# Kernel optimization log

Measured on AMD Instinct MI355X. Metric: run time of the kernel, lower is better.

Reference implementation:

```python
import jax, jax.numpy as jnp
import numpy as np

NUM_HOPS = 3

def _position_encoding(sentence_size, embedding_size):
    # Vectorized version of the double loop in the source.
    i = np.arange(1, embedding_size + 1, dtype=np.float32)[:, None]  # [E,1]
    j = np.arange(1, sentence_size + 1, dtype=np.float32)[None, :]   # [1,S]
    enc = (i - embedding_size / 2.0) * (j - sentence_size / 2.0)
    enc = 1.0 + 4.0 * enc / embedding_size / sentence_size
    return jnp.asarray(np.transpose(enc))  # [S, E]

def setup_inputs() -> dict:
    key = jax.random.key(0)
    ks = jax.random.split(key, 9)
    B, M, S, E, V, OUT = 16, 512, 32, 128, 32000, 128
    scale = 0.02
    return {
        "queries": jax.random.randint(ks[0], (B, S), 0, V, dtype=jnp.int32),
        "stories": jax.random.randint(ks[1], (B, M, S), 0, V, dtype=jnp.int32),
        "query_biases": jax.random.normal(ks[2], (V - 1, E), jnp.float32) * scale,
        "stories_biases": jax.random.normal(ks[3], (V - 1, E), jnp.float32) * scale,
        "memory_biases": jax.random.normal(ks[4], (M, E), jnp.float32) * scale,
        "output_biases": jax.random.normal(ks[5], (V - 1, E), jnp.float32) * scale,
        "w_intermediate": jax.random.normal(ks[6], (E, E), jnp.float32) * scale,
        "w_output": jax.random.normal(ks[7], (E, OUT), jnp.float32) * scale,
        "w_final": jax.random.normal(ks[8], (OUT, V), jnp.float32) * scale,
    }

def reference(queries, stories, query_biases, stories_biases, memory_biases,
              output_biases, w_intermediate, w_output, w_final):
    B, M, S = stories.shape
    E = query_biases.shape[1]
    enc = _position_encoding(S, E)  # [S, E]
    nil = jnp.zeros((1, E), dtype=query_biases.dtype)

    # Story memory: gather -> positional weight -> reduce over sentence axis.
    st_tab = jnp.concatenate([stories_biases, nil], axis=0)          # [V, E]
    mem_emb = st_tab[stories]                                        # [B,M,S,E]
    memory = jnp.einsum('bmse,se->bme', mem_emb, enc) + memory_biases

    # Query embedding.
    q_tab = jnp.concatenate([query_biases, nil], axis=0)
    q = jnp.einsum('bse,se->be', q_tab[queries], enc)                # [B,E]

    # Output memory.
    o_tab = jnp.concatenate([output_biases, nil], axis=0)
    output = jnp.einsum('bmse,se->bme', o_tab[stories], enc)         # [B,M,E]

    out_layer = q
    for hop in range(NUM_HOPS):
        probs = jax.nn.softmax(jnp.einsum('bme,be->bm', memory, q))  # [B,M]
        layer_out = jnp.einsum('bme,bm->be', output, probs)          # [B,E]
        w = w_output if hop == NUM_HOPS - 1 else w_intermediate
        out_layer = (q + layer_out) @ w
        q = out_layer                     # pre-nonlinearity state, as in source
        out_layer = jax.nn.relu(out_layer)

    return out_layer @ w_final            # [B, vocab]
```

## Files before the change

kernel.cpp:

```cpp
#include <hip/hip_runtime.h>

constexpr int kB  = 16;
constexpr int kM  = 512;
constexpr int kS  = 32;
constexpr int kE  = 128;
constexpr int kV  = 32000;
constexpr int kVN = kV - 1;
constexpr int kMS = 132;

__global__ __launch_bounds__(256) void embed_stories_kernel(
    const int*   __restrict__ stories,
    const float* __restrict__ st_bias,
    const float* __restrict__ out_bias,
    const float* __restrict__ mem_bias,
    float*       __restrict__ memory,
    float*       __restrict__ output,
    unsigned*    __restrict__ bar)
{
    __shared__ int sidx[2][kS];
    __shared__ __align__(16) float pm[8][kE];
    __shared__ __align__(16) float po[8][kE];

    const int t    = threadIdx.x;
    const int row0 = blockIdx.x * 2;
    if (t < 64) sidx[t >> 5][t & 31] = stories[row0 * kS + t];
    if (blockIdx.x == 0 && t < kB) bar[t] = 0u;
    __syncthreads();

    const int g    = t >> 5;
    const int lane = t & 31;
    const int p    = g >> 2;
    const int ph   = g & 3;
    const int e0   = lane * 4;
    const float ef0 = (float)(e0 - 63), ef1 = (float)(e0 - 62);
    const float ef2 = (float)(e0 - 61), ef3 = (float)(e0 - 60);

    float4 am = {0.f, 0.f, 0.f, 0.f};
    float4 ao = {0.f, 0.f, 0.f, 0.f};
    #pragma unroll
    for (int j = 0; j < 8; ++j) {
        const int s   = ph * 8 + j;
        const int idx = sidx[p][s];
        const int ci  = idx < kVN ? idx : (kVN - 1);
        const float live = (idx < kVN) ? 1.0f : 0.0f;
        const float sf = (float)(s - 15) * (1.0f / 1024.0f);
        const float4 vm = *(const float4*)(st_bias  + (size_t)ci * kE + e0);
        const float4 vo = *(const float4*)(out_bias + (size_t)ci * kE + e0);
        const float c0 = fmaf(ef0, sf, 1.0f) * live;
        const float c1 = fmaf(ef1, sf, 1.0f) * live;
        const float c2 = fmaf(ef2, sf, 1.0f) * live;
        const float c3 = fmaf(ef3, sf, 1.0f) * live;
        am.x = fmaf(vm.x, c0, am.x); am.y = fmaf(vm.y, c1, am.y);
        am.z = fmaf(vm.z, c2, am.z); am.w = fmaf(vm.w, c3, am.w);
        ao.x = fmaf(vo.x, c0, ao.x); ao.y = fmaf(vo.y, c1, ao.y);
        ao.z = fmaf(vo.z, c2, ao.z); ao.w = fmaf(vo.w, c3, ao.w);
    }
    *(float4*)&pm[g][e0] = am;
    *(float4*)&po[g][e0] = ao;
    __syncthreads();

    const int pr = t >> 7;
    const int e  = t & 127;
    const int row = row0 + pr;
    const int m   = row & (kM - 1);
    const float sm = pm[pr * 4 + 0][e] + pm[pr * 4 + 1][e] +
                     pm[pr * 4 + 2][e] + pm[pr * 4 + 3][e];
    const float so = po[pr * 4 + 0][e] + po[pr * 4 + 1][e] +
                     po[pr * 4 + 2][e] + po[pr * 4 + 3][e];
    memory[(size_t)row * kE + e] = sm + mem_bias[m * kE + e];
    output[(size_t)row * kE + e] = so;
}

__device__ __forceinline__ void group_barrier(unsigned* ctr, unsigned target)
{
    __syncthreads();
    if (threadIdx.x == 0) {
        __hip_atomic_fetch_add(ctr, 1u, __ATOMIC_RELEASE, __HIP_MEMORY_SCOPE_AGENT);
        while (__hip_atomic_load(ctr, __ATOMIC_RELAXED, __HIP_MEMORY_SCOPE_AGENT) < target)
            __builtin_amdgcn_s_sleep(2);
    }
    __syncthreads();
}
__device__ __forceinline__ void cstore(float* p, float v) {
    __hip_atomic_store(p, v, __ATOMIC_RELAXED, __HIP_MEMORY_SCOPE_AGENT);
}
__device__ __forceinline__ float cload(const float* p) {
    return __hip_atomic_load(p, __ATOMIC_RELAXED, __HIP_MEMORY_SCOPE_AGENT);
}

__global__ __launch_bounds__(1024) void hops_kernel(
    const int*   __restrict__ queries,
    const float* __restrict__ q_bias,
    const float* __restrict__ memory,
    const float* __restrict__ output,
    const float* __restrict__ w_int,
    const float* __restrict__ w_out,
    float*       __restrict__ numer,
    float*       __restrict__ denom,
    float*       __restrict__ xg,
    unsigned*    __restrict__ bar)
{
    __shared__ __align__(16) float mem_lds[128 * kMS];
    __shared__ __align__(16) float out_lds[128 * kE];
    __shared__ float sc_q[128];
    __shared__ __align__(16) float q_s[kE];
    __shared__ float xb[kE];
    __shared__ __align__(16) float part8[8][kE];
    __shared__ int qidx[kS];

    const int bid = blockIdx.x;
    const int b   = bid & 15;
    const int qtr = bid >> 4;
    const int t   = threadIdx.x;
    unsigned* ctr = bar + b;

    const float* memb = memory + ((size_t)b * kM + qtr * 128) * kE;
    const float* outb = output + ((size_t)b * kM + qtr * 128) * kE;
    #pragma unroll
    for (int i = 0; i < 4; ++i) {
        const int flat = t + i * 1024;
        const int rr = flat >> 5, ff = (flat & 31) * 4;
        *(float4*)&mem_lds[rr * kMS + ff] = *(const float4*)&memb[(size_t)rr * kE + ff];
        *(float4*)&out_lds[rr * kE  + ff] = *(const float4*)&outb[(size_t)rr * kE + ff];
    }
    if (t < kS) qidx[t] = queries[b * kS + t];
    __syncthreads();

    if (t < 256) {
        const int g = t >> 5, lane = t & 31, e0 = lane * 4;
        const float f0 = (float)(e0 - 63) * (1.0f / 1024.0f);
        const float f1 = (float)(e0 - 62) * (1.0f / 1024.0f);
        const float f2 = (float)(e0 - 61) * (1.0f / 1024.0f);
        const float f3 = (float)(e0 - 60) * (1.0f / 1024.0f);
        float4 a = {0.f, 0.f, 0.f, 0.f};
        #pragma unroll
        for (int j = 0; j < 4; ++j) {
            const int s   = g * 4 + j;
            const int idx = qidx[s];
            const int ci  = idx < kVN ? idx : (kVN - 1);
            const float live = (idx < kVN) ? 1.0f : 0.0f;
            const float sf = (float)(s - 15);
            const float4 v = *(const float4*)&q_bias[(size_t)ci * kE + e0];
            a.x = fmaf(v.x, fmaf(f0, sf, 1.f) * live, a.x);
            a.y = fmaf(v.y, fmaf(f1, sf, 1.f) * live, a.y);
            a.z = fmaf(v.z, fmaf(f2, sf, 1.f) * live, a.z);
            a.w = fmaf(v.w, fmaf(f3, sf, 1.f) * live, a.w);
        }
        *(float4*)&part8[g][e0] = a;
    }
    __syncthreads();
    if (t < kE) {
        float s = 0.f;
        #pragma unroll
        for (int g = 0; g < 8; ++g) s += part8[g][t];
        q_s[t] = s;
    }
    __syncthreads();

    const int grp = t >> 7;
    const int e   = t & 127;

    for (int hop = 0; hop < 3; ++hop) {
        {
            const int rw = t >> 3, sub = t & 7;
            const float4* qv = (const float4*)&q_s[sub * 16];
            const float4* mv = (const float4*)&mem_lds[rw * kMS + sub * 16];
            float d = 0.f;
            #pragma unroll
            for (int i = 0; i < 4; ++i) {
                const float4 m4 = mv[i], q4 = qv[i];
                d = fmaf(m4.x, q4.x, d); d = fmaf(m4.y, q4.y, d);
                d = fmaf(m4.z, q4.z, d); d = fmaf(m4.w, q4.w, d);
            }
            d += __shfl_down(d, 4);
            d += __shfl_down(d, 2);
            d += __shfl_down(d, 1);
            if (sub == 0) sc_q[rw] = __expf(d);
        }
        __syncthreads();

        {
            float acc = 0.f;
            const float* pp = &sc_q[grp * 16];
            const float* ob = &out_lds[grp * 16 * kE + e];
            #pragma unroll
            for (int j = 0; j < 16; ++j)
                acc = fmaf(pp[j], ob[j * kE], acc);
            part8[grp][e] = acc;
        }
        __syncthreads();

        const int pb = hop & 1;
        float* nq = numer + (((size_t)pb * kB + b) * 4 + qtr) * kE;
        if (t < kE) {
            float s = 0.f;
            #pragma unroll
            for (int g = 0; g < 8; ++g) s += part8[g][t];
            cstore(&nq[t], s);
        } else if (t < 192) {
            const int l = t - 128;
            float s2 = sc_q[l] + sc_q[l + 64];
            #pragma unroll
            for (int off = 32; off; off >>= 1) s2 += __shfl_down(s2, off);
            if (l == 0) cstore(&denom[((size_t)pb * kB + b) * 4 + qtr], s2);
        }

        group_barrier(ctr, 4u * (hop + 1));

        if (t < kE) {
            const float* nn = numer + ((size_t)pb * kB + b) * 4 * kE;
            const float* dd = denom + ((size_t)pb * kB + b) * 4;
            const float ns = cload(&nn[t]) + cload(&nn[kE + t]) +
                             cload(&nn[2 * kE + t]) + cload(&nn[3 * kE + t]);
            const float ds = cload(&dd[0]) + cload(&dd[1]) +
                             cload(&dd[2]) + cload(&dd[3]);
            xb[t] = q_s[t] + ns / ds;
        }
        __syncthreads();

        {
            const float* w = (hop == 2) ? w_out : w_int;
            float acc = 0.f;
            #pragma unroll
            for (int j = 0; j < 16; ++j) {
                const int k = grp * 16 + j;
                acc = fmaf(xb[k], w[k * kE + e], acc);
            }
            part8[grp][e] = acc;
        }
        __syncthreads();
        if (t < kE) {
            float s = 0.f;
            #pragma unroll
            for (int g = 0; g < 8; ++g) s += part8[g][t];
            q_s[t] = s;
        }
        __syncthreads();
    }

    if (qtr == 0 && t < kE) xg[t * kB + b] = fmaxf(q_s[t], 0.f);
}

__global__ __launch_bounds__(256) void final_kernel(
    const float* __restrict__ xg,
    const float* __restrict__ wf,
    float*       __restrict__ out)
{
    __shared__ float ps[128 * kB];
    const int t = threadIdx.x;
    const int v = blockIdx.x * 128 + (t & 127);
    const int h = t >> 7;

    float acc[kB];
    #pragma unroll
    for (int b = 0; b < kB; ++b) acc[b] = 0.f;

    const int e0 = h * 64;
    #pragma unroll 4
    for (int ei = 0; ei < 64; ++ei) {
        const int e = e0 + ei;
        const float wv = wf[(size_t)e * kV + v];
        const float* xr = xg + e * kB;
        #pragma unroll
        for (int b = 0; b < kB; ++b) acc[b] = fmaf(xr[b], wv, acc[b]);
    }
    if (h == 1) {
        #pragma unroll
        for (int b = 0; b < kB; ++b) ps[(t & 127) * kB + b] = acc[b];
    }
    __syncthreads();
    if (h == 0) {
        #pragma unroll
        for (int b = 0; b < kB; ++b)
            out[(size_t)b * kV + v] = acc[b] + ps[(t & 127) * kB + b];
    }
}

extern "C" void kernel_launch(void* const* d_in, const int* in_sizes, int n_in,
                              void* d_out, int out_size, void* d_ws, size_t ws_size,
                              hipStream_t stream)
{
    const int*   queries  = (const int*)  d_in[0];
    const int*   stories  = (const int*)  d_in[1];
    const float* q_bias   = (const float*)d_in[2];
    const float* st_bias  = (const float*)d_in[3];
    const float* mem_bias = (const float*)d_in[4];
    const float* out_bias = (const float*)d_in[5];
    const float* w_int    = (const float*)d_in[6];
    const float* w_out    = (const float*)d_in[7];
    const float* w_final  = (const float*)d_in[8];
    float* out = (float*)d_out;

    float* memory = (float*)d_ws;
    float* output = memory + (size_t)kB * kM * kE;
    float* numer  = output + (size_t)kB * kM * kE;
    float* denom  = numer  + 2 * kB * 4 * kE;
    float* xg     = denom  + 2 * kB * 4;
    unsigned* bar = (unsigned*)(xg + kE * kB);

    embed_stories_kernel<<<dim3((kB * kM) / 2), dim3(256), 0, stream>>>(
        stories, st_bias, out_bias, mem_bias, memory, output, bar);

    hops_kernel<<<dim3(64), dim3(1024), 0, stream>>>(
        queries, q_bias, memory, output, w_int, w_out,
        numer, denom, xg, bar);

    final_kernel<<<dim3(kV / 128), dim3(256), 0, stream>>>(xg, w_final, out);
}
```

Before: 161.5 us.

## Fuse final vocab projection into hops kernel via grid-wide barrier

Merges the final [B,128]x[128,V] projection into the persistent hops kernel. A global atomic barrier over all 64 blocks waits for xg, and then each block computes 500 vocab columns with 1024 threads. This removes one kernel launch and the gap between launches. The cost is that the projection now runs on only 64 workgroups instead of 250, so less parallelism is available for the memory-bound w_final read (16 MB). The query index staging in LDS is also dropped in favour of direct global reads.

```diff
diff --git a/kernel.cpp b/kernel.cpp
--- a/kernel.cpp
+++ b/kernel.cpp
@@ -24,7 +24,7 @@
     const int t    = threadIdx.x;
     const int row0 = blockIdx.x * 2;
     if (t < 64) sidx[t >> 5][t & 31] = stories[row0 * kS + t];
-    if (blockIdx.x == 0 && t < kB) bar[t] = 0u;
+    if (blockIdx.x == 0 && t < kB + 1) bar[t] = 0u;
     __syncthreads();
 
     const int g    = t >> 5;
@@ -88,17 +88,19 @@
     return __hip_atomic_load(p, __ATOMIC_RELAXED, __HIP_MEMORY_SCOPE_AGENT);
 }
 
-__global__ __launch_bounds__(1024) void hops_kernel(
+__global__ __launch_bounds__(1024) void hops_final_kernel(
     const int*   __restrict__ queries,
     const float* __restrict__ q_bias,
     const float* __restrict__ memory,
     const float* __restrict__ output,
     const float* __restrict__ w_int,
     const float* __restrict__ w_out,
+    const float* __restrict__ wf,
     float*       __restrict__ numer,
     float*       __restrict__ denom,
-    float*       __restrict__ xg,
-    unsigned*    __restrict__ bar)
+    float*                    xg,
+    unsigned*    __restrict__ bar,
+    float*       __restrict__ out)
 {
     __shared__ __align__(16) float mem_lds[128 * kMS];
     __shared__ __align__(16) float out_lds[128 * kE];
@@ -106,7 +108,6 @@
     __shared__ __align__(16) float q_s[kE];
     __shared__ float xb[kE];
     __shared__ __align__(16) float part8[8][kE];
-    __shared__ int qidx[kS];
 
     const int bid = blockIdx.x;
     const int b   = bid & 15;
@@ -123,8 +124,6 @@
         *(float4*)&mem_lds[rr * kMS + ff] = *(const float4*)&memb[(size_t)rr * kE + ff];
         *(float4*)&out_lds[rr * kE  + ff] = *(const float4*)&outb[(size_t)rr * kE + ff];
     }
-    if (t < kS) qidx[t] = queries[b * kS + t];
-    __syncthreads();
 
     if (t < 256) {
         const int g = t >> 5, lane = t & 31, e0 = lane * 4;
@@ -136,7 +135,7 @@
         #pragma unroll
         for (int j = 0; j < 4; ++j) {
             const int s   = g * 4 + j;
-            const int idx = qidx[s];
+            const int idx = queries[b * kS + s];
             const int ci  = idx < kVN ? idx : (kVN - 1);
             const float live = (idx < kVN) ? 1.0f : 0.0f;
             const float sf = (float)(s - 15);
@@ -238,41 +237,40 @@
         __syncthreads();
     }
 
-    if (qtr == 0 && t < kE) xg[t * kB + b] = fmaxf(q_s[t], 0.f);
-}
-
-__global__ __launch_bounds__(256) void final_kernel(
-    const float* __restrict__ xg,
-    const float* __restrict__ wf,
-    float*       __restrict__ out)
-{
-    __shared__ float ps[128 * kB];
-    const int t = threadIdx.x;
-    const int v = blockIdx.x * 128 + (t & 127);
-    const int h = t >> 7;
-
-    float acc[kB];
-    #pragma unroll
-    for (int b = 0; b < kB; ++b) acc[b] = 0.f;
-
-    const int e0 = h * 64;
-    #pragma unroll 4
-    for (int ei = 0; ei < 64; ++ei) {
-        const int e = e0 + ei;
-        const float wv = wf[(size_t)e * kV + v];
-        const float* xr = xg + e * kB;
+    if (qtr == 0 && t < kE) cstore(&xg[t * kB + b], fmaxf(q_s[t], 0.f));
+    group_barrier(bar + kB, 64u);
+
+    {
+        const int vt = t & 511;
+        const int h  = t >> 9;
+        const int v  = bid * 500 + vt;
+        float* ps = out_lds;
+        float acc[kB];
         #pragma unroll
-        for (int b = 0; b < kB; ++b) acc[b] = fmaf(xr[b], wv, acc[b]);
-    }
-    if (h == 1) {
-        #pragma unroll
-        for (int b = 0; b < kB; ++b) ps[(t & 127) * kB + b] = acc[b];
-    }
-    __syncthreads();
-    if (h == 0) {
-        #pragma unroll
-        for (int b = 0; b < kB; ++b)
-            out[(size_t)b * kV + v] = acc[b] + ps[(t & 127) * kB + b];
+        for (int b2 = 0; b2 < kB; ++b2) acc[b2] = 0.f;
+
+        if (vt < 500) {
+            const int e0 = h * 64;
+            #pragma unroll 8
+            for (int ei = 0; ei < 64; ++ei) {
+                const int e = e0 + ei;
+                const float wv = wf[(size_t)e * kV + v];
+                const float* xr = xg + e * kB;
+                #pragma unroll
+                for (int b2 = 0; b2 < kB; ++b2)
+                    acc[b2] = fmaf(xr[b2], wv, acc[b2]);
+            }
+            if (h == 1) {
+                #pragma unroll
+                for (int b2 = 0; b2 < kB; ++b2) ps[b2 * 512 + vt] = acc[b2];
+            }
+        }
+        __syncthreads();
+        if (h == 0 && vt < 500) {
+            #pragma unroll
+            for (int b2 = 0; b2 < kB; ++b2)
+                out[(size_t)b2 * kV + v] = acc[b2] + ps[b2 * 512 + vt];
+        }
     }
 }
 
@@ -301,9 +299,7 @@
     embed_stories_kernel<<<dim3((kB * kM) / 2), dim3(256), 0, stream>>>(
         stories, st_bias, out_bias, mem_bias, memory, output, bar);
 
-    hops_kernel<<<dim3(64), dim3(1024), 0, stream>>>(
-        queries, q_bias, memory, output, w_int, w_out,
-        numer, denom, xg, bar);
-
-    final_kernel<<<dim3(kV / 128), dim3(256), 0, stream>>>(xg, w_final, out);
-}
+    hops_final_kernel<<<dim3(64), dim3(1024), 0, stream>>>(
+        queries, q_bias, memory, output, w_int, w_out, w_final,
+        numer, denom, xg, bar, out);
+}
```

Measured after the change: 201.1 us. 1.24x slower.

## Collapse hops kernel to one block per batch, dropping cross-block barrier

Applied to the files above, without the earlier changes.

Replaces the four-blocks-per-batch hops kernel, which used global atomic counters and spin-wait barriers to combine partial softmax numerators and denominators, with a single 1024-thread block per batch. Each block reads memory and output rows directly from global memory (L2) every hop instead of staging them in LDS, and computes the softmax denominator locally. This removes inter-block synchronisation, atomic traffic and the barrier reset. In exchange it uses only 16 workgroups, so far fewer CUs share the per-hop reads of 512x128 rows.

```diff
diff --git a/kernel.cpp b/kernel.cpp
--- a/kernel.cpp
+++ b/kernel.cpp
@@ -1,12 +1,11 @@
 #include <hip/hip_runtime.h>
 
-constexpr int kB  = 16;
-constexpr int kM  = 512;
-constexpr int kS  = 32;
-constexpr int kE  = 128;
-constexpr int kV  = 32000;
-constexpr int kVN = kV - 1;
-constexpr int kMS = 132;
+constexpr int kB    = 16;
+constexpr int kM    = 512;
+constexpr int kS    = 32;
+constexpr int kE    = 128;
+constexpr int kV    = 32000;
+constexpr int kVN   = kV - 1;
 
 __global__ __launch_bounds__(256) void embed_stories_kernel(
     const int*   __restrict__ stories,
@@ -14,8 +13,7 @@
     const float* __restrict__ out_bias,
     const float* __restrict__ mem_bias,
     float*       __restrict__ memory,
-    float*       __restrict__ output,
-    unsigned*    __restrict__ bar)
+    float*       __restrict__ output)
 {
     __shared__ int sidx[2][kS];
     __shared__ __align__(16) float pm[8][kE];
@@ -24,7 +22,6 @@
     const int t    = threadIdx.x;
     const int row0 = blockIdx.x * 2;
     if (t < 64) sidx[t >> 5][t & 31] = stories[row0 * kS + t];
-    if (blockIdx.x == 0 && t < kB) bar[t] = 0u;
     __syncthreads();
 
     const int g    = t >> 5;
@@ -71,60 +68,25 @@
     output[(size_t)row * kE + e] = so;
 }
 
-__device__ __forceinline__ void group_barrier(unsigned* ctr, unsigned target)
-{
-    __syncthreads();
-    if (threadIdx.x == 0) {
-        __hip_atomic_fetch_add(ctr, 1u, __ATOMIC_RELEASE, __HIP_MEMORY_SCOPE_AGENT);
-        while (__hip_atomic_load(ctr, __ATOMIC_RELAXED, __HIP_MEMORY_SCOPE_AGENT) < target)
-            __builtin_amdgcn_s_sleep(2);
-    }
-    __syncthreads();
-}
-__device__ __forceinline__ void cstore(float* p, float v) {
-    __hip_atomic_store(p, v, __ATOMIC_RELAXED, __HIP_MEMORY_SCOPE_AGENT);
-}
-__device__ __forceinline__ float cload(const float* p) {
-    return __hip_atomic_load(p, __ATOMIC_RELAXED, __HIP_MEMORY_SCOPE_AGENT);
-}
-
-__global__ __launch_bounds__(1024) void hops_kernel(
+__global__ __launch_bounds__(1024) void hops16_kernel(
     const int*   __restrict__ queries,
     const float* __restrict__ q_bias,
     const float* __restrict__ memory,
     const float* __restrict__ output,
     const float* __restrict__ w_int,
     const float* __restrict__ w_out,
-    float*       __restrict__ numer,
-    float*       __restrict__ denom,
-    float*       __restrict__ xg,
-    unsigned*    __restrict__ bar)
-{
-    __shared__ __align__(16) float mem_lds[128 * kMS];
-    __shared__ __align__(16) float out_lds[128 * kE];
-    __shared__ float sc_q[128];
+    float*       __restrict__ xg)
+{
+    __shared__ __align__(16) float part8[8][kE];
+    __shared__ float sc[kM];
     __shared__ __align__(16) float q_s[kE];
     __shared__ float xb[kE];
-    __shared__ __align__(16) float part8[8][kE];
-    __shared__ int qidx[kS];
-
-    const int bid = blockIdx.x;
-    const int b   = bid & 15;
-    const int qtr = bid >> 4;
-    const int t   = threadIdx.x;
-    unsigned* ctr = bar + b;
-
-    const float* memb = memory + ((size_t)b * kM + qtr * 128) * kE;
-    const float* outb = output + ((size_t)b * kM + qtr * 128) * kE;
-    #pragma unroll
-    for (int i = 0; i < 4; ++i) {
-        const int flat = t + i * 1024;
-        const int rr = flat >> 5, ff = (flat & 31) * 4;
-        *(float4*)&mem_lds[rr * kMS + ff] = *(const float4*)&memb[(size_t)rr * kE + ff];
-        *(float4*)&out_lds[rr * kE  + ff] = *(const float4*)&outb[(size_t)rr * kE + ff];
-    }
-    if (t < kS) qidx[t] = queries[b * kS + t];
-    __syncthreads();
+    __shared__ float ds_s;
+
+    const int b = blockIdx.x;
+    const int t = threadIdx.x;
+    const float* memb = memory + (size_t)b * kM * kE;
+    const float* outb = output + (size_t)b * kM * kE;
 
     if (t < 256) {
         const int g = t >> 5, lane = t & 31, e0 = lane * 4;
@@ -136,7 +98,7 @@
         #pragma unroll
         for (int j = 0; j < 4; ++j) {
             const int s   = g * 4 + j;
-            const int idx = qidx[s];
+            const int idx = queries[b * kS + s];
             const int ci  = idx < kVN ? idx : (kVN - 1);
             const float live = (idx < kVN) ? 1.0f : 0.0f;
             const float sf = (float)(s - 15);
@@ -157,68 +119,53 @@
     }
     __syncthreads();
 
-    const int grp = t >> 7;
-    const int e   = t & 127;
-
     for (int hop = 0; hop < 3; ++hop) {
         {
-            const int rw = t >> 3, sub = t & 7;
-            const float4* qv = (const float4*)&q_s[sub * 16];
-            const float4* mv = (const float4*)&mem_lds[rw * kMS + sub * 16];
+            const int rw = t >> 1, h = t & 1;
+            const float4* mv = (const float4*)(memb + (size_t)rw * kE + h * 64);
+            const float4* qv = (const float4*)(q_s + h * 64);
             float d = 0.f;
             #pragma unroll
-            for (int i = 0; i < 4; ++i) {
+            for (int i = 0; i < 16; ++i) {
                 const float4 m4 = mv[i], q4 = qv[i];
                 d = fmaf(m4.x, q4.x, d); d = fmaf(m4.y, q4.y, d);
                 d = fmaf(m4.z, q4.z, d); d = fmaf(m4.w, q4.w, d);
             }
-            d += __shfl_down(d, 4);
-            d += __shfl_down(d, 2);
-            d += __shfl_down(d, 1);
-            if (sub == 0) sc_q[rw] = __expf(d);
-        }
-        __syncthreads();
+            d += __shfl_xor(d, 1);
+            if (h == 0) sc[rw] = __expf(d);
+        }
+        __syncthreads();
+
+        if (t < 64) {
+            float s = 0.f;
+            #pragma unroll
+            for (int j = 0; j < 8; ++j) s += sc[t + 64 * j];
+            #pragma unroll
+            for (int off = 32; off; off >>= 1) s += __shfl_down(s, off);
+            if (t == 0) ds_s = s;
+        }
 
         {
+            const int grp = t >> 7, e = t & 127;
+            const float* og = outb + (size_t)grp * 64 * kE + e;
             float acc = 0.f;
-            const float* pp = &sc_q[grp * 16];
-            const float* ob = &out_lds[grp * 16 * kE + e];
-            #pragma unroll
-            for (int j = 0; j < 16; ++j)
-                acc = fmaf(pp[j], ob[j * kE], acc);
+            #pragma unroll 16
+            for (int j = 0; j < 64; ++j)
+                acc = fmaf(sc[grp * 64 + j], og[j * kE], acc);
             part8[grp][e] = acc;
         }
         __syncthreads();
 
-        const int pb = hop & 1;
-        float* nq = numer + (((size_t)pb * kB + b) * 4 + qtr) * kE;
         if (t < kE) {
-            float s = 0.f;
-            #pragma unroll
-            for (int g = 0; g < 8; ++g) s += part8[g][t];
-            cstore(&nq[t], s);
-        } else if (t < 192) {
-            const int l = t - 128;
-            float s2 = sc_q[l] + sc_q[l + 64];
-            #pragma unroll
-            for (int off = 32; off; off >>= 1) s2 += __shfl_down(s2, off);
-            if (l == 0) cstore(&denom[((size_t)pb * kB + b) * 4 + qtr], s2);
-        }
-
-        group_barrier(ctr, 4u * (hop + 1));
-
-        if (t < kE) {
-            const float* nn = numer + ((size_t)pb * kB + b) * 4 * kE;
-            const float* dd = denom + ((size_t)pb * kB + b) * 4;
-            const float ns = cload(&nn[t]) + cload(&nn[kE + t]) +
-                             cload(&nn[2 * kE + t]) + cload(&nn[3 * kE + t]);
-            const float ds = cload(&dd[0]) + cload(&dd[1]) +
-                             cload(&dd[2]) + cload(&dd[3]);
-            xb[t] = q_s[t] + ns / ds;
+            float ns = 0.f;
+            #pragma unroll
+            for (int g = 0; g < 8; ++g) ns += part8[g][t];
+            xb[t] = q_s[t] + ns / ds_s;
         }
         __syncthreads();
 
         {
+            const int grp = t >> 7, e = t & 127;
             const float* w = (hop == 2) ? w_out : w_int;
             float acc = 0.f;
             #pragma unroll
@@ -238,7 +185,7 @@
         __syncthreads();
     }
 
-    if (qtr == 0 && t < kE) xg[t * kB + b] = fmaxf(q_s[t], 0.f);
+    if (t < kE) xg[t * kB + b] = fmaxf(q_s[t], 0.f);
 }
 
 __global__ __launch_bounds__(256) void final_kernel(
@@ -293,17 +240,13 @@
 
     float* memory = (float*)d_ws;
     float* output = memory + (size_t)kB * kM * kE;
-    float* numer  = output + (size_t)kB * kM * kE;
-    float* denom  = numer  + 2 * kB * 4 * kE;
-    float* xg     = denom  + 2 * kB * 4;
-    unsigned* bar = (unsigned*)(xg + kE * kB);
+    float* xg     = output + (size_t)kB * kM * kE;
 
     embed_stories_kernel<<<dim3((kB * kM) / 2), dim3(256), 0, stream>>>(
-        stories, st_bias, out_bias, mem_bias, memory, output, bar);
-
-    hops_kernel<<<dim3(64), dim3(1024), 0, stream>>>(
-        queries, q_bias, memory, output, w_int, w_out,
-        numer, denom, xg, bar);
+        stories, st_bias, out_bias, mem_bias, memory, output);
+
+    hops16_kernel<<<dim3(kB), dim3(1024), 0, stream>>>(
+        queries, q_bias, memory, output, w_int, w_out, xg);
 
     final_kernel<<<dim3(kV / 128), dim3(256), 0, stream>>>(xg, w_final, out);
 }
```

Result: slower. 196.4 us (+21.6%).
